# Optimization experiments

Hardware: AMD Instinct MI355X
Metric: run time of the kernel (lower is better)

## Reference

```python
import jax, jax.numpy as jnp
import numpy as np

VOCAB, BLOCK, D, H, L = 50257, 2048, 768, 12, 4
B, T = 1, 2048
DH = D // H


def setup_inputs() -> dict:
    key = jax.random.key(0)
    ks = jax.random.split(key, 16)
    s = 0.02
    return {
        "tokens": jax.random.randint(ks[0], (B, T), 0, VOCAB),
        "wte": jax.random.normal(ks[1], (VOCAB, D), jnp.float32) * s,
        "wpe": jax.random.normal(ks[2], (BLOCK, D), jnp.float32) * s,
        "ln1_w": jnp.ones((L, D), jnp.float32),
        "ln1_b": jnp.zeros((L, D), jnp.float32),
        "qkv_w": jax.random.normal(ks[3], (L, D, 3 * D), jnp.float32) * s,
        "qkv_b": jnp.zeros((L, 3 * D), jnp.float32),
        "proj_w": jax.random.normal(ks[4], (L, D, D), jnp.float32) * s,
        "proj_b": jnp.zeros((L, D), jnp.float32),
        "ln2_w": jnp.ones((L, D), jnp.float32),
        "ln2_b": jnp.zeros((L, D), jnp.float32),
        "fc_w": jax.random.normal(ks[5], (L, D, 4 * D), jnp.float32) * s,
        "fc_b": jnp.zeros((L, 4 * D), jnp.float32),
        "fcp_w": jax.random.normal(ks[6], (L, 4 * D, D), jnp.float32) * s,
        "fcp_b": jnp.zeros((L, D), jnp.float32),
        "lnf_w": jnp.ones((D,), jnp.float32),
        "lnf_b": jnp.zeros((D,), jnp.float32),
    }


def _ln(x, w, b, eps=1e-5):
    m = jnp.mean(x, axis=-1, keepdims=True)
    v = jnp.mean((x - m) ** 2, axis=-1, keepdims=True)
    return (x - m) * jax.lax.rsqrt(v + eps) * w + b


def _attn(x, wq, bq, wp, bp):
    Bq, Tq, _ = x.shape
    qkv = x @ wq + bq  # [B,T,3D]
    q, k, v = jnp.split(qkv, 3, axis=-1)
    q = q.reshape(Bq, Tq, H, DH).transpose(0, 2, 1, 3)  # [B,H,T,dh]
    k = k.reshape(Bq, Tq, H, DH).transpose(0, 2, 1, 3)
    v = v.reshape(Bq, Tq, H, DH).transpose(0, 2, 1, 3)
    w = jnp.einsum("bhqd,bhkd->bhqk", q, k) / np.sqrt(DH).astype(np.float32)
    mask = jnp.tril(jnp.ones((Tq, Tq), bool))
    w = jnp.where(mask, w, -jnp.inf)
    w = jax.nn.softmax(w, axis=-1)
    y = jnp.einsum("bhqk,bhkd->bhqd", w, v)
    y = y.transpose(0, 2, 1, 3).reshape(Bq, Tq, D)
    return y @ wp + bp


def reference(tokens, wte, wpe, ln1_w, ln1_b, qkv_w, qkv_b, proj_w, proj_b,
              ln2_w, ln2_b, fc_w, fc_b, fcp_w, fcp_b, lnf_w, lnf_b):
    x = wte[tokens] + wpe[jnp.arange(tokens.shape[1])]  # [B,T,D]
    for l in range(L):
        x = x + _attn(_ln(x, ln1_w[l], ln1_b[l]), qkv_w[l], qkv_b[l], proj_w[l], proj_b[l])
        h = _ln(x, ln2_w[l], ln2_b[l]) @ fc_w[l] + fc_b[l]
        h = jax.nn.gelu(h, approximate=True)
        x = x + h @ fcp_w[l] + fcp_b[l]
    x = _ln(x, lnf_w, lnf_b)
    logits = x @ wte.T  # tied lm_head, [B,T,V]
    return logits
```

## Files before the change

### kernel.cpp

```cpp
#include <hip/hip_runtime.h>
#include <hip/hip_bf16.h>

#define TSEQ   2048
#define DMODEL 768
#define NHEAD  12
#define DHEAD  64
#define NLAYER 4
#define VOCAB  50257
#define VPAD   50304

typedef __attribute__((ext_vector_type(8))) short short8;
typedef __attribute__((ext_vector_type(4))) float f32x4;
typedef unsigned short ushort_t;

union F8 { short8 v; unsigned long long q[2]; };

__device__ __forceinline__ float b2f(ushort_t u) {
  return __uint_as_float(((unsigned)u) << 16);
}
__device__ __forceinline__ ushort_t f2bu(float f) {
  unsigned u = __float_as_uint(f);
  unsigned r = (u + 0x7fffu + ((u >> 16) & 1u)) >> 16;
  return (ushort_t)r;
}

__device__ __forceinline__ void gload_lds16(const void* g, void* l) {
  __builtin_amdgcn_global_load_lds(
      (const __attribute__((address_space(1))) unsigned int*)g,
      (__attribute__((address_space(3))) unsigned int*)l, 16, 0, 0);
}

__global__ __launch_bounds__(256) void embed_kernel(
    const int* __restrict__ tok, const float* __restrict__ wte,
    const float* __restrict__ wpe, float* __restrict__ x) {
  int i = blockIdx.x * 256 + threadIdx.x;
  int t = i / DMODEL;
  int d = i - t * DMODEL;
  x[i] = wte[tok[t] * DMODEL + d] + wpe[i];
}

__global__ __launch_bounds__(256) void cvt_kernel(
    const float* __restrict__ in, ushort_t* __restrict__ out, int n4) {
  for (int i = blockIdx.x * 256 + threadIdx.x; i < n4; i += gridDim.x * 256) {
    float4 f = reinterpret_cast<const float4*>(in)[i];
    ushort4 o;
    o.x = f2bu(f.x); o.y = f2bu(f.y); o.z = f2bu(f.z); o.w = f2bu(f.w);
    reinterpret_cast<ushort4*>(out)[i] = o;
  }
}

__global__ __launch_bounds__(256) void tcvt_kernel(
    const float* __restrict__ W, ushort_t* __restrict__ Wt, int K, int N,
    long long wstride) {
  W  += (size_t)blockIdx.z * wstride;
  Wt += (size_t)blockIdx.z * wstride;
  __shared__ float Ts[32][33];
  int n0 = blockIdx.x * 32, k0 = blockIdx.y * 32;
  int tx = threadIdx.x & 31, ty = threadIdx.x >> 5;
#pragma unroll
  for (int s = 0; s < 4; ++s)
    Ts[ty + 8 * s][tx] = W[(size_t)(k0 + ty + 8 * s) * N + n0 + tx];
  __syncthreads();
#pragma unroll
  for (int s = 0; s < 4; ++s)
    Wt[(size_t)(n0 + ty + 8 * s) * K + k0 + tx] = f2bu(Ts[tx][ty + 8 * s]);
}

__global__ __launch_bounds__(256) void ln_kernel(
    const float* __restrict__ x, const float* __restrict__ w,
    const float* __restrict__ b, ushort_t* __restrict__ out) {
  int row = blockIdx.x;
  int t = threadIdx.x;
  const float* xr = x + row * DMODEL;
  float v0 = xr[t], v1 = xr[t + 256], v2 = xr[t + 512];
  float s = v0 + v1 + v2;
  float q = v0 * v0 + v1 * v1 + v2 * v2;
#pragma unroll
  for (int off = 32; off >= 1; off >>= 1) {
    s += __shfl_xor(s, off);
    q += __shfl_xor(q, off);
  }
  __shared__ float rs[4], rq[4];
  int wid = t >> 6;
  if ((t & 63) == 0) { rs[wid] = s; rq[wid] = q; }
  __syncthreads();
  s = rs[0] + rs[1] + rs[2] + rs[3];
  q = rq[0] + rq[1] + rq[2] + rq[3];
  float mean = s * (1.f / DMODEL);
  float var  = q * (1.f / DMODEL) - mean * mean;
  float rstd = rsqrtf(var + 1e-5f);
  ushort_t* o = out + row * DMODEL;
  o[t]       = f2bu((v0 - mean) * rstd * w[t]       + b[t]);
  o[t + 256] = f2bu((v1 - mean) * rstd * w[t + 256] + b[t + 256]);
  o[t + 512] = f2bu((v2 - mean) * rstd * w[t + 512] + b[t + 512]);
}

template <int TM, int TN, bool BIAS, bool RES, bool GELU, bool OUTBF16, bool XSWZ>
__global__ __launch_bounds__(256) void mm_kernel(
    const ushort_t* __restrict__ A, const ushort_t* __restrict__ Bt,
    const float* __restrict__ bias, const float* __restrict__ res,
    void* __restrict__ outp, int N, int K, int nrowblk, int nwg) {
  constexpr int HM = TM / 2, HN = TN / 2, FI = TM / 32, FJ = TN / 32;
  constexpr int NCA = TM / 32, NCB = TN / 32;
  __shared__ ushort_t Asm[TM * 64];
  __shared__ ushort_t Bsm[TN * 64];
  const int tid = threadIdx.x;
  const int lane = tid & 63, wid = tid >> 6;
  const int wr = wid >> 1, wc = wid & 1;
  const int l15 = lane & 15, c4 = lane >> 4;
  const int qb0 = (c4 >> 1) << 4;
  const int qb1 = qb0 + 32;
  const int e8 = (c4 & 1) * 8;

  int bid = blockIdx.x;
  if (XSWZ) { int q = nwg >> 3; bid = (bid & 7) * q + (bid >> 3); }
  const int rowb = bid % nrowblk, colb = bid / nrowblk;
  const int rowA0 = rowb * TM, colB0 = colb * TN;

  int ap0[FI], ax[FI], bp0[FJ], bx[FJ];
#pragma unroll
  for (int i = 0; i < FI; ++i) {
    int r = wr * HM + i * 16 + l15;
    ap0[i] = r * 128 + e8; ax[i] = (r & 7) << 4;
  }
#pragma unroll
  for (int j = 0; j < FJ; ++j) {
    int r = wc * HN + j * 16 + l15;
    bp0[j] = r * 128 + e8; bx[j] = (r & 7) << 4;
  }

  const ushort_t* asrc[NCA]; ushort_t* adst[NCA];
  const ushort_t* bsrc[NCB]; ushort_t* bdst[NCB];
#pragma unroll
  for (int s = 0; s < NCA; ++s) {
    int ci = tid + s * 256;
    int row = ci >> 3;
    int logch = (ci & 7) ^ (row & 7);
    asrc[s] = A + (size_t)(rowA0 + row) * K + logch * 8;
    adst[s] = Asm + ci * 8;
  }
#pragma unroll
  for (int s = 0; s < NCB; ++s) {
    int ci = tid + s * 256;
    int row = ci >> 3;
    int logch = (ci & 7) ^ (row & 7);
    bsrc[s] = Bt + (size_t)(colB0 + row) * K + logch * 8;
    bdst[s] = Bsm + ci * 8;
  }

  f32x4 acc[FI][FJ] = {};
  const char* Ab = (const char*)Asm;
  const char* Bb = (const char*)Bsm;

  for (int kt = 0; kt < K; kt += 64) {
    __syncthreads();
#pragma unroll
    for (int s = 0; s < NCA; ++s) gload_lds16(asrc[s] + kt, adst[s]);
#pragma unroll
    for (int s = 0; s < NCB; ++s) gload_lds16(bsrc[s] + kt, bdst[s]);
    __syncthreads();
#pragma unroll
    for (int kk = 0; kk < 2; ++kk) {
      const int k64 = kk * 64;
      short8 a[FI], b[FJ];
#pragma unroll
      for (int i = 0; i < FI; ++i) {
        F8 f;
        f.q[0] = *(const unsigned long long*)(Ab + ap0[i] + ((k64 + qb0) ^ ax[i]));
        f.q[1] = *(const unsigned long long*)(Ab + ap0[i] + ((k64 + qb1) ^ ax[i]));
        a[i] = f.v;
      }
#pragma unroll
      for (int j = 0; j < FJ; ++j) {
        F8 f;
        f.q[0] = *(const unsigned long long*)(Bb + bp0[j] + ((k64 + qb0) ^ bx[j]));
        f.q[1] = *(const unsigned long long*)(Bb + bp0[j] + ((k64 + qb1) ^ bx[j]));
        b[j] = f.v;
      }
#pragma unroll
      for (int i = 0; i < FI; ++i)
#pragma unroll
        for (int j = 0; j < FJ; ++j)
          acc[i][j] = __builtin_amdgcn_mfma_f32_16x16x32_bf16(a[i], b[j], acc[i][j], 0, 0, 0);
    }
  }

#pragma unroll
  for (int i = 0; i < FI; ++i) {
    const int rbase = rowA0 + wr * HM + i * 16 + c4 * 4;
#pragma unroll
    for (int j = 0; j < FJ; ++j) {
      const int col = colB0 + wc * HN + j * 16 + l15;
      if (col < N) {
        float bv = BIAS ? bias[col] : 0.f;
#pragma unroll
        for (int t = 0; t < 4; ++t) {
          float v = acc[i][j][t] + bv;
          if (GELU) {
            float z = 1.5957691216057308f * (v + 0.044715f * v * v * v);
            float th = 1.f - 2.f / (__expf(z) + 1.f);
            v = 0.5f * v * (1.f + th);
          }
          size_t o = (size_t)(rbase + t) * N + col;
          if (RES)          ((float*)outp)[o] = v + res[o];
          else if (OUTBF16) ((ushort_t*)outp)[o] = f2bu(v);
          else              ((float*)outp)[o] = v;
        }
      }
    }
  }
}

__global__ __launch_bounds__(256) void fattn_kernel(
    const ushort_t* __restrict__ qkv, ushort_t* __restrict__ y) {
  const int id = blockIdx.x;
  const int w32 = id / NHEAD;
  const int h = id - w32 * NHEAD;
  const int qb = (w32 & 1) ? (w32 >> 1) : (31 - (w32 >> 1));
  const int q0 = qb * 64;

  __shared__ ushort_t Ksm[64 * 64];
  __shared__ ushort_t Vsm[64 * 64];
  __shared__ ushort_t Psm[4 * 16 * 64];

  const int tid = threadIdx.x;
  const int lane = tid & 63, wv = tid >> 6;
  const int l15 = lane & 15, c4 = lane >> 4;
  const int r7 = l15 & 7;

  const ushort_t* qrow = qkv + (size_t)(q0 + wv * 16 + l15) * (3 * DMODEL) + h * DHEAD;
  const short8 qf0 = *(const short8*)(qrow + c4 * 8);
  const short8 qf1 = *(const short8*)(qrow + 32 + c4 * 8);

  const ushort_t* ksrc[2]; ushort_t* kdst[2];
#pragma unroll
  for (int s = 0; s < 2; ++s) {
    int row = wv * 16 + s * 8 + (lane >> 3);
    int cs = (lane & 7) ^ (row & 7);
    ksrc[s] = qkv + (size_t)row * (3 * DMODEL) + DMODEL + h * DHEAD + cs * 8;
    kdst[s] = Ksm + ((wv * 2 + s) * 64) * 8;
  }
  const int vk = tid & 63, vd0 = (tid >> 6) * 8;
  const ushort_t* vsrc = qkv + (size_t)vk * (3 * DMODEL) + 2 * DMODEL + h * DHEAD;
  const int vkoff = ((vk >> 3) << 3) + (vk & 7);

  float m[4] = {-1e30f, -1e30f, -1e30f, -1e30f};
  float l[4] = {};
  f32x4 acc[4] = {};
  ushort_t* Pw = Psm + wv * 1024;

  for (int k0 = 0; k0 <= q0; k0 += 64) {
    const size_t koff = (size_t)k0 * (3 * DMODEL);
    short8 v0 = *(const short8*)(vsrc + koff + vd0);
    short8 v1 = *(const short8*)(vsrc + koff + vd0 + 32);
    __syncthreads();
#pragma unroll
    for (int s = 0; s < 2; ++s) gload_lds16(ksrc[s] + koff, kdst[s]);
#pragma unroll
    for (int j = 0; j < 8; ++j) {
      int d = vd0 + j;
      Vsm[d * 64 + (vkoff ^ ((d & 7) << 3))] = (ushort_t)v0[j];
      int d2 = d + 32;
      Vsm[d2 * 64 + (vkoff ^ ((d2 & 7) << 3))] = (ushort_t)v1[j];
    }
    __syncthreads();

    f32x4 sv[4];
#pragma unroll
    for (int kt = 0; kt < 4; ++kt) {
      const ushort_t* krow = Ksm + (kt * 16 + l15) * 64;
      short8 kb0 = *(const short8*)(krow + ((c4 ^ r7) << 3));
      short8 kb1 = *(const short8*)(krow + (((4 + c4) ^ r7) << 3));
      f32x4 s = {};
      s = __builtin_amdgcn_mfma_f32_16x16x32_bf16(qf0, kb0, s, 0, 0, 0);
      s = __builtin_amdgcn_mfma_f32_16x16x32_bf16(qf1, kb1, s, 0, 0, 0);
      sv[kt] = s * 0.125f;
    }
    if (k0 == q0) {
#pragma unroll
      for (int kt = 0; kt < 4; ++kt)
#pragma unroll
        for (int r = 0; r < 4; ++r)
          if (kt * 16 + l15 > wv * 16 + c4 * 4 + r) sv[kt][r] = -1e30f;
    }

#pragma unroll
    for (int r = 0; r < 4; ++r) {
      float mv = fmaxf(fmaxf(sv[0][r], sv[1][r]), fmaxf(sv[2][r], sv[3][r]));
      mv = fmaxf(mv, __shfl_xor(mv, 1));
      mv = fmaxf(mv, __shfl_xor(mv, 2));
      mv = fmaxf(mv, __shfl_xor(mv, 4));
      mv = fmaxf(mv, __shfl_xor(mv, 8));
      float nm = fmaxf(m[r], mv);
      float sc = __expf(m[r] - nm);
      m[r] = nm;
      const int row = c4 * 4 + r;
      float sum = 0.f;
#pragma unroll
      for (int kt = 0; kt < 4; ++kt) {
        float p = __expf(sv[kt][r] - nm);
        sum += p;
        Pw[row * 64 + (((kt * 2 + (l15 >> 3)) ^ (row & 7)) << 3) + (l15 & 7)] = f2bu(p);
      }
      sum += __shfl_xor(sum, 1);
      sum += __shfl_xor(sum, 2);
      sum += __shfl_xor(sum, 4);
      sum += __shfl_xor(sum, 8);
      l[r] = l[r] * sc + sum;
#pragma unroll
      for (int j = 0; j < 4; ++j) acc[j][r] *= sc;
    }

    const ushort_t* prow = Pw + l15 * 64;
    short8 pa0 = *(const short8*)(prow + ((c4 ^ r7) << 3));
    short8 pa1 = *(const short8*)(prow + (((4 + c4) ^ r7) << 3));
#pragma unroll
    for (int j = 0; j < 4; ++j) {
      const ushort_t* vrow = Vsm + (j * 16 + l15) * 64;
      short8 vb0 = *(const short8*)(vrow + ((c4 ^ r7) << 3));
      short8 vb1 = *(const short8*)(vrow + (((4 + c4) ^ r7) << 3));
      acc[j] = __builtin_amdgcn_mfma_f32_16x16x32_bf16(pa0, vb0, acc[j], 0, 0, 0);
      acc[j] = __builtin_amdgcn_mfma_f32_16x16x32_bf16(pa1, vb1, acc[j], 0, 0, 0);
    }
  }

  float inv[4];
#pragma unroll
  for (int r = 0; r < 4; ++r) inv[r] = 1.f / l[r];
#pragma unroll
  for (int j = 0; j < 4; ++j)
#pragma unroll
    for (int r = 0; r < 4; ++r)
      y[(size_t)(q0 + wv * 16 + c4 * 4 + r) * DMODEL + h * DHEAD + j * 16 + l15] =
          f2bu(acc[j][r] * inv[r]);
}

extern "C" void kernel_launch(void* const* d_in, const int* in_sizes, int n_in,
                              void* d_out, int out_size, void* d_ws, size_t ws_size,
                              hipStream_t stream) {
  const int*   tokens = (const int*)d_in[0];
  const float* wte    = (const float*)d_in[1];
  const float* wpe    = (const float*)d_in[2];
  const float* ln1_w  = (const float*)d_in[3];
  const float* ln1_b  = (const float*)d_in[4];
  const float* qkv_w  = (const float*)d_in[5];
  const float* qkv_b  = (const float*)d_in[6];
  const float* proj_w = (const float*)d_in[7];
  const float* proj_b = (const float*)d_in[8];
  const float* ln2_w  = (const float*)d_in[9];
  const float* ln2_b  = (const float*)d_in[10];
  const float* fc_w   = (const float*)d_in[11];
  const float* fc_b   = (const float*)d_in[12];
  const float* fcp_w  = (const float*)d_in[13];
  const float* fcp_b  = (const float*)d_in[14];
  const float* lnf_w  = (const float*)d_in[15];
  const float* lnf_b  = (const float*)d_in[16];
  float* out = (float*)d_out;

  char* p = (char*)d_ws;
  auto alloc = [&](size_t bytes) { char* r = p; p += (bytes + 255) & ~(size_t)255; return r; };
  float*    x     = (float*)alloc((size_t)TSEQ * DMODEL * 4);
  ushort_t* lnb   = (ushort_t*)alloc((size_t)TSEQ * DMODEL * 2);
  ushort_t* buf   = (ushort_t*)alloc((size_t)TSEQ * 4 * DMODEL * 2);
  ushort_t* wteb  = (ushort_t*)alloc((size_t)VPAD * DMODEL * 2);
  ushort_t* qkvwt = (ushort_t*)alloc((size_t)NLAYER * 3 * DMODEL * DMODEL * 2);
  ushort_t* projwt= (ushort_t*)alloc((size_t)NLAYER * DMODEL * DMODEL * 2);
  ushort_t* fcwt  = (ushort_t*)alloc((size_t)NLAYER * 4 * DMODEL * DMODEL * 2);
  ushort_t* fcpwt = (ushort_t*)alloc((size_t)NLAYER * 4 * DMODEL * DMODEL * 2);
  ushort_t* qkvb  = buf;
  ushort_t* yb    = buf + (size_t)TSEQ * 3 * DMODEL;
  ushort_t* hfcb  = buf;

  dim3 b256(256);

  hipMemsetAsync(wteb + (size_t)VOCAB * DMODEL, 0,
                 (size_t)(VPAD - VOCAB) * DMODEL * 2, stream);
  cvt_kernel<<<dim3(4096), b256, 0, stream>>>(wte, wteb, VOCAB * DMODEL / 4);
  tcvt_kernel<<<dim3(3 * DMODEL / 32, DMODEL / 32, NLAYER), b256, 0, stream>>>(
      qkv_w, qkvwt, DMODEL, 3 * DMODEL, (long long)3 * DMODEL * DMODEL);
  tcvt_kernel<<<dim3(DMODEL / 32, DMODEL / 32, NLAYER), b256, 0, stream>>>(
      proj_w, projwt, DMODEL, DMODEL, (long long)DMODEL * DMODEL);
  tcvt_kernel<<<dim3(4 * DMODEL / 32, DMODEL / 32, NLAYER), b256, 0, stream>>>(
      fc_w, fcwt, DMODEL, 4 * DMODEL, (long long)4 * DMODEL * DMODEL);
  tcvt_kernel<<<dim3(DMODEL / 32, 4 * DMODEL / 32, NLAYER), b256, 0, stream>>>(
      fcp_w, fcpwt, 4 * DMODEL, DMODEL, (long long)4 * DMODEL * DMODEL);

  embed_kernel<<<dim3(TSEQ * DMODEL / 256), b256, 0, stream>>>(tokens, wte, wpe, x);

  for (int l = 0; l < NLAYER; ++l) {
    ln_kernel<<<dim3(TSEQ), b256, 0, stream>>>(x, ln1_w + l * DMODEL, ln1_b + l * DMODEL, lnb);
    mm_kernel<64, 128, true, false, false, true, false><<<dim3(32 * 18), b256, 0, stream>>>(
        lnb, qkvwt + (size_t)l * 3 * DMODEL * DMODEL, qkv_b + (size_t)l * 3 * DMODEL,
        nullptr, qkvb, 3 * DMODEL, DMODEL, 32, 576);
    fattn_kernel<<<dim3(32 * NHEAD), b256, 0, stream>>>(qkvb, yb);
    mm_kernel<64, 64, true, true, false, false, false><<<dim3(12 * 32), b256, 0, stream>>>(
        yb, projwt + (size_t)l * DMODEL * DMODEL, proj_b + (size_t)l * DMODEL,
        x, x, DMODEL, DMODEL, 32, 384);
    ln_kernel<<<dim3(TSEQ), b256, 0, stream>>>(x, ln2_w + l * DMODEL, ln2_b + l * DMODEL, lnb);
    mm_kernel<64, 128, true, false, true, true, false><<<dim3(32 * 24), b256, 0, stream>>>(
        lnb, fcwt + (size_t)l * 4 * DMODEL * DMODEL, fc_b + (size_t)l * 4 * DMODEL,
        nullptr, hfcb, 4 * DMODEL, DMODEL, 32, 768);
    mm_kernel<64, 64, true, true, false, false, false><<<dim3(12 * 32), b256, 0, stream>>>(
        hfcb, fcpwt + (size_t)l * DMODEL * 4 * DMODEL, fcp_b + (size_t)l * DMODEL,
        x, x, DMODEL, 4 * DMODEL, 32, 384);
  }

  ln_kernel<<<dim3(TSEQ), b256, 0, stream>>>(x, lnf_w, lnf_b, lnb);
  mm_kernel<128, 128, false, false, false, false, true><<<dim3(393 * 16), b256, 0, stream>>>(
      lnb, wteb, nullptr, nullptr, out, VOCAB, DMODEL, 16, 393 * 16);
}
```

Measured before the change: 1.049 ms.

## Double-buffer K tiles and prefetch V in flash attention loop

```diff
diff --git a/kernel.cpp b/kernel.cpp
--- a/kernel.cpp
+++ b/kernel.cpp
@@ -219,7 +219,7 @@
   const int qb = (w32 & 1) ? (w32 >> 1) : (31 - (w32 >> 1));
   const int q0 = qb * 64;
 
-  __shared__ ushort_t Ksm[64 * 64];
+  __shared__ ushort_t Ksm[2][64 * 64];
   __shared__ ushort_t Vsm[64 * 64];
   __shared__ ushort_t Psm[4 * 16 * 64];
 
@@ -232,13 +232,13 @@
   const short8 qf0 = *(const short8*)(qrow + c4 * 8);
   const short8 qf1 = *(const short8*)(qrow + 32 + c4 * 8);
 
-  const ushort_t* ksrc[2]; ushort_t* kdst[2];
+  const ushort_t* ksrc[2]; int kdoff[2];
 #pragma unroll
   for (int s = 0; s < 2; ++s) {
     int row = wv * 16 + s * 8 + (lane >> 3);
     int cs = (lane & 7) ^ (row & 7);
     ksrc[s] = qkv + (size_t)row * (3 * DMODEL) + DMODEL + h * DHEAD + cs * 8;
-    kdst[s] = Ksm + ((wv * 2 + s) * 64) * 8;
+    kdoff[s] = ((wv * 2 + s) * 64) * 8;
   }
   const int vk = tid & 63, vd0 = (tid >> 6) * 8;
   const ushort_t* vsrc = qkv + (size_t)vk * (3 * DMODEL) + 2 * DMODEL + h * DHEAD;
@@ -248,27 +248,37 @@
   float l[4] = {};
   f32x4 acc[4] = {};
   ushort_t* Pw = Psm + wv * 1024;
-
-  for (int k0 = 0; k0 <= q0; k0 += 64) {
-    const size_t koff = (size_t)k0 * (3 * DMODEL);
-    short8 v0 = *(const short8*)(vsrc + koff + vd0);
-    short8 v1 = *(const short8*)(vsrc + koff + vd0 + 32);
-    __syncthreads();
-#pragma unroll
-    for (int s = 0; s < 2; ++s) gload_lds16(ksrc[s] + koff, kdst[s]);
+  const int nt = qb + 1;
+
+  short8 vA0, vA1, vB0, vB1;
+#pragma unroll
+  for (int s = 0; s < 2; ++s) gload_lds16(ksrc[s], &Ksm[0][kdoff[s]]);
+  vA0 = *(const short8*)(vsrc + vd0);
+  vA1 = *(const short8*)(vsrc + vd0 + 32);
+
+  auto body = [&](int t, short8& cv0, short8& cv1, short8& nv0, short8& nv1) {
+    const int p = t & 1;
+    const int k0 = t * 64;
+    asm volatile("s_waitcnt vmcnt(0)" ::: "memory");
+    __builtin_amdgcn_s_barrier();
 #pragma unroll
     for (int j = 0; j < 8; ++j) {
       int d = vd0 + j;
-      Vsm[d * 64 + (vkoff ^ ((d & 7) << 3))] = (ushort_t)v0[j];
+      Vsm[d * 64 + (vkoff ^ ((d & 7) << 3))] = (ushort_t)cv0[j];
       int d2 = d + 32;
-      Vsm[d2 * 64 + (vkoff ^ ((d2 & 7) << 3))] = (ushort_t)v1[j];
-    }
-    __syncthreads();
-
+      Vsm[d2 * 64 + (vkoff ^ ((d2 & 7) << 3))] = (ushort_t)cv1[j];
+    }
+    if (t + 1 < nt) {
+      const size_t koff = (size_t)(k0 + 64) * (3 * DMODEL);
+#pragma unroll
+      for (int s = 0; s < 2; ++s) gload_lds16(ksrc[s] + koff, &Ksm[p ^ 1][kdoff[s]]);
+      nv0 = *(const short8*)(vsrc + koff + vd0);
+      nv1 = *(const short8*)(vsrc + koff + vd0 + 32);
+    }
     f32x4 sv[4];
 #pragma unroll
     for (int kt = 0; kt < 4; ++kt) {
-      const ushort_t* krow = Ksm + (kt * 16 + l15) * 64;
+      const ushort_t* krow = &Ksm[p][(kt * 16 + l15) * 64];
       short8 kb0 = *(const short8*)(krow + ((c4 ^ r7) << 3));
       short8 kb1 = *(const short8*)(krow + (((4 + c4) ^ r7) << 3));
       f32x4 s = {};
@@ -283,7 +293,6 @@
         for (int r = 0; r < 4; ++r)
           if (kt * 16 + l15 > wv * 16 + c4 * 4 + r) sv[kt][r] = -1e30f;
     }
-
 #pragma unroll
     for (int r = 0; r < 4; ++r) {
       float mv = fmaxf(fmaxf(sv[0][r], sv[1][r]), fmaxf(sv[2][r], sv[3][r]));
@@ -298,9 +307,9 @@
       float sum = 0.f;
 #pragma unroll
       for (int kt = 0; kt < 4; ++kt) {
-        float p = __expf(sv[kt][r] - nm);
-        sum += p;
-        Pw[row * 64 + (((kt * 2 + (l15 >> 3)) ^ (row & 7)) << 3) + (l15 & 7)] = f2bu(p);
+        float ppp = __expf(sv[kt][r] - nm);
+        sum += ppp;
+        Pw[row * 64 + (((kt * 2 + (l15 >> 3)) ^ (row & 7)) << 3) + (l15 & 7)] = f2bu(ppp);
       }
       sum += __shfl_xor(sum, 1);
       sum += __shfl_xor(sum, 2);
@@ -310,7 +319,9 @@
 #pragma unroll
       for (int j = 0; j < 4; ++j) acc[j][r] *= sc;
     }
-
+    asm volatile("s_waitcnt lgkmcnt(0)" ::: "memory");
+    __builtin_amdgcn_s_barrier();
+    __builtin_amdgcn_sched_barrier(0);
     const ushort_t* prow = Pw + l15 * 64;
     short8 pa0 = *(const short8*)(prow + ((c4 ^ r7) << 3));
     short8 pa1 = *(const short8*)(prow + (((4 + c4) ^ r7) << 3));
@@ -322,6 +333,11 @@
       acc[j] = __builtin_amdgcn_mfma_f32_16x16x32_bf16(pa0, vb0, acc[j], 0, 0, 0);
       acc[j] = __builtin_amdgcn_mfma_f32_16x16x32_bf16(pa1, vb1, acc[j], 0, 0, 0);
     }
+  };
+
+  for (int t = 0; t < nt; ++t) {
+    if (t & 1) body(t, vB0, vB1, vA0, vA1);
+    else       body(t, vA0, vA1, vB0, vB1);
   }
 
   float inv[4];
```

Measured after the change: 1.075 ms. +2.5%, slower.
